# Kernel tuning notes

Hardware: AMD Instinct MI355X
Metric: run time of the kernel (lower is better)

The kernel has to match this reference:

```python
import jax, jax.numpy as jnp
import numpy as np

EPS = 1e-10


def setup_inputs() -> dict:
    key = jax.random.key(0)
    k1, k2, k3 = jax.random.split(key, 3)
    B, X, Y = 16, 512, 512
    predictions = jax.random.uniform(k1, (B, 5, X, Y), dtype=jnp.float32)
    inputs = jax.random.uniform(k2, (B, 3, X, Y), dtype=jnp.float32)
    heart = jax.random.randint(k3, (B, 1, X, Y), 0, 2, dtype=jnp.int32)
    return {"predictions": predictions, "inputs": inputs, "heart": heart}


def reference(predictions, inputs, heart):
    # predictions: [B,5,X,Y] soft class maps (chan 0 unused); inputs: [B,3,X,Y] MRI modalities
    # heart: [B,1,X,Y] binary ROI mask. Loops over b/k/m in the torch source are vectorized;
    # boolean-mask gathers become multiply-by-mask with masked reductions (same math).
    mask = (heart[:, 0] == 1).astype(predictions.dtype)          # [B,X,Y]
    pred = predictions[:, 1:5]                                   # [B,K=4,X,Y]
    inp = inputs                                                 # [B,M=3,X,Y]

    w = pred * mask[:, None]                                     # masked soft weights [B,K,X,Y]
    sw = jnp.sum(w, axis=(2, 3))                                 # [B,K]
    denom = sw[:, :, None] + EPS                                 # [B,K,1]

    # per-(k,m) weighted mean over masked pixels
    mu = jnp.einsum('bkxy,bmxy->bkm', w, inp) / denom            # [B,K,M]
    diff = inp[:, None, :, :, :] - mu[:, :, :, None, None]       # [B,K,M,X,Y]
    var = jnp.einsum('bkxy,bkmxy->bkm', w, diff * diff) / denom + EPS

    # Gaussian pdf per (k,m,pixel), scaled by pred_k (as in temp[k,m] = pred[k]*pdf)
    inv_norm = 1.0 / jnp.sqrt(2.0 * jnp.pi * var)                # [B,K,M]
    pdf = inv_norm[:, :, :, None, None] * jnp.exp(
        -(diff * diff) / (2.0 * var)[:, :, :, None, None])      # [B,K,M,X,Y]
    temp = pred[:, :, None] * pdf                                # [B,K,M,X,Y]

    mix = jnp.sum(jnp.prod(temp, axis=2), axis=1)                # [B,X,Y]
    loglik = jnp.log(mix + EPS)                                  # [B,X,Y]

    # masked mean over ROI pixels per batch (== torch.mean over gathered pixels)
    per_b = -jnp.sum(loglik * mask, axis=(1, 2)) / jnp.sum(mask, axis=(1, 2))
    return jnp.mean(per_b)
```

## Files before the change

kernel.cpp:

```cpp
#include <hip/hip_runtime.h>
#include <math.h>

constexpr int NB = 16;
constexpr int XY = 512 * 512;
constexpr int NV = XY / 4;
constexpr int G  = 128;

constexpr int P1OFF = 4096;

__device__ __forceinline__ float waveReduce64(float v) {
#pragma unroll
    for (int off = 32; off > 0; off >>= 1) v += __shfl_down(v, off, 64);
    return v;
}

__device__ __forceinline__ float rfl(float x) {
    return __uint_as_float(__builtin_amdgcn_readfirstlane(__float_as_uint(x)));
}

#define PIX1(h_, e0_, e1_, e2_, p0_, p1_, p2_, p3_) do {                      \
    float mm_ = ((h_) == 1) ? 1.f : 0.f;                                      \
    cnt += mm_;                                                               \
    float w0_ = (p0_) * mm_, w1_ = (p1_) * mm_, w2_ = (p2_) * mm_,            \
          w3_ = (p3_) * mm_;                                                  \
    s0_0 += w0_; s0_1 += w1_; s0_2 += w2_; s0_3 += w3_;                       \
    float t_;                                                                 \
    t_ = w0_ * (e0_); u00 += t_; q00 = fmaf(t_, (e0_), q00);                  \
    t_ = w0_ * (e1_); u01 += t_; q01 = fmaf(t_, (e1_), q01);                  \
    t_ = w0_ * (e2_); u02 += t_; q02 = fmaf(t_, (e2_), q02);                  \
    t_ = w1_ * (e0_); u10 += t_; q10 = fmaf(t_, (e0_), q10);                  \
    t_ = w1_ * (e1_); u11 += t_; q11 = fmaf(t_, (e1_), q11);                  \
    t_ = w1_ * (e2_); u12 += t_; q12 = fmaf(t_, (e2_), q12);                  \
    t_ = w2_ * (e0_); u20 += t_; q20 = fmaf(t_, (e0_), q20);                  \
    t_ = w2_ * (e1_); u21 += t_; q21 = fmaf(t_, (e1_), q21);                  \
    t_ = w2_ * (e2_); u22 += t_; q22 = fmaf(t_, (e2_), q22);                  \
    t_ = w3_ * (e0_); u30 += t_; q30 = fmaf(t_, (e0_), q30);                  \
    t_ = w3_ * (e1_); u31 += t_; q31 = fmaf(t_, (e1_), q31);                  \
    t_ = w3_ * (e2_); u32 += t_; q32 = fmaf(t_, (e2_), q32);                  \
} while (0)

#define RED(i_, var_) { float r_ = waveReduce64(var_); if (lane == 0) sh[wav][i_] = r_; }

#define PARAMK(K_, mu0_, mu1_, mu2_, h0_, h1_, h2_, C_) {                     \
    double S0_ = tot[1 + (K_)];                                               \
    double den_ = S0_ + 1e-10;                                                \
    double Cd_ = 1.0;                                                         \
    double S1_, S2_, muv_, var_;                                              \
    S1_ = tot[5 + (K_)*3 + 0]; S2_ = tot[17 + (K_)*3 + 0];                    \
    muv_ = S1_ / den_;                                                        \
    var_ = (S2_ - 2.0 * muv_ * S1_ + muv_ * muv_ * S0_) / den_ + 1e-10;       \
    mu0_ = (float)muv_; h0_ = (float)(0.5 / var_);                            \
    Cd_ *= 1.0 / sqrt(6.283185307179586 * var_);                              \
    S1_ = tot[5 + (K_)*3 + 1]; S2_ = tot[17 + (K_)*3 + 1];                    \
    muv_ = S1_ / den_;                                                        \
    var_ = (S2_ - 2.0 * muv_ * S1_ + muv_ * muv_ * S0_) / den_ + 1e-10;       \
    mu1_ = (float)muv_; h1_ = (float)(0.5 / var_);                            \
    Cd_ *= 1.0 / sqrt(6.283185307179586 * var_);                              \
    S1_ = tot[5 + (K_)*3 + 2]; S2_ = tot[17 + (K_)*3 + 2];                    \
    muv_ = S1_ / den_;                                                        \
    var_ = (S2_ - 2.0 * muv_ * S1_ + muv_ * muv_ * S0_) / den_ + 1e-10;       \
    mu2_ = (float)muv_; h2_ = (float)(0.5 / var_);                            \
    Cd_ *= 1.0 / sqrt(6.283185307179586 * var_);                              \
    C_ = (float)Cd_;                                                          \
}

#define PIX2(h_, e0_, e1_, e2_, p0_, p1_, p2_, p3_) do {                      \
    float m_ = ((h_) == 1) ? 1.f : 0.f;                                       \
    float d0_, d1_, d2_, ex_, pc_;                                            \
    float mix_;                                                               \
    d0_ = (e0_) - mu00; d1_ = (e1_) - mu01; d2_ = (e2_) - mu02;               \
    ex_ = fmaf(d0_ * d0_, hv00, fmaf(d1_ * d1_, hv01, d2_ * d2_ * hv02));     \
    pc_ = (p0_) * (p0_) * (p0_);                                              \
    mix_ = C0 * pc_ * __expf(-ex_);                                           \
    d0_ = (e0_) - mu10; d1_ = (e1_) - mu11; d2_ = (e2_) - mu12;               \
    ex_ = fmaf(d0_ * d0_, hv10, fmaf(d1_ * d1_, hv11, d2_ * d2_ * hv12));     \
    pc_ = (p1_) * (p1_) * (p1_);                                              \
    mix_ = fmaf(C1 * pc_, __expf(-ex_), mix_);                                \
    d0_ = (e0_) - mu20; d1_ = (e1_) - mu21; d2_ = (e2_) - mu22;               \
    ex_ = fmaf(d0_ * d0_, hv20, fmaf(d1_ * d1_, hv21, d2_ * d2_ * hv22));     \
    pc_ = (p2_) * (p2_) * (p2_);                                              \
    mix_ = fmaf(C2 * pc_, __expf(-ex_), mix_);                                \
    d0_ = (e0_) - mu30; d1_ = (e1_) - mu31; d2_ = (e2_) - mu32;               \
    ex_ = fmaf(d0_ * d0_, hv30, fmaf(d1_ * d1_, hv31, d2_ * d2_ * hv32));     \
    pc_ = (p3_) * (p3_) * (p3_);                                              \
    mix_ = fmaf(C3 * pc_, __expf(-ex_), mix_);                                \
    lacc += m_ * __logf(mix_ + 1e-10f);                                       \
} while (0)

#define LOADSET1(S, v_)                                                       \
    int4   h##S  = H[v_];                                                     \
    float4 f0##S = I0[v_], f1##S = I1[v_], f2##S = I2[v_];                    \
    float4 g0##S = P1[v_], g1##S = P2[v_], g2##S = P3[v_], g3##S = P4[v_];

#define PIXSET1(S)                                                            \
    PIX1(h##S.x, f0##S.x, f1##S.x, f2##S.x, g0##S.x, g1##S.x, g2##S.x, g3##S.x); \
    PIX1(h##S.y, f0##S.y, f1##S.y, f2##S.y, g0##S.y, g1##S.y, g2##S.y, g3##S.y); \
    PIX1(h##S.z, f0##S.z, f1##S.z, f2##S.z, g0##S.z, g1##S.z, g2##S.z, g3##S.z); \
    PIX1(h##S.w, f0##S.w, f1##S.w, f2##S.w, g0##S.w, g1##S.w, g2##S.w, g3##S.w);

#define PIXSET2(S)                                                            \
    PIX2(h##S.x, f0##S.x, f1##S.x, f2##S.x, g0##S.x, g1##S.x, g2##S.x, g3##S.x); \
    PIX2(h##S.y, f0##S.y, f1##S.y, f2##S.y, g0##S.y, g1##S.y, g2##S.y, g3##S.y); \
    PIX2(h##S.z, f0##S.z, f1##S.z, f2##S.z, g0##S.z, g1##S.z, g2##S.z, g3##S.z); \
    PIX2(h##S.w, f0##S.w, f1##S.w, f2##S.w, g0##S.w, g1##S.w, g2##S.w, g3##S.w);

#define DECL_PTRS                                                             \
    const float4* P1 = reinterpret_cast<const float4*>(predictions + (size_t)b * 5 * XY + 1 * XY); \
    const float4* P2 = reinterpret_cast<const float4*>(predictions + (size_t)b * 5 * XY + 2 * XY); \
    const float4* P3 = reinterpret_cast<const float4*>(predictions + (size_t)b * 5 * XY + 3 * XY); \
    const float4* P4 = reinterpret_cast<const float4*>(predictions + (size_t)b * 5 * XY + 4 * XY); \
    const float4* I0 = reinterpret_cast<const float4*>(inputs + (size_t)b * 3 * XY + 0 * XY); \
    const float4* I1 = reinterpret_cast<const float4*>(inputs + (size_t)b * 3 * XY + 1 * XY); \
    const float4* I2 = reinterpret_cast<const float4*>(inputs + (size_t)b * 3 * XY + 2 * XY); \
    const int4*   H  = reinterpret_cast<const int4*>(heart + (size_t)b * XY);

__global__ __launch_bounds__(256, 2) void pass1_moments(
        const float* __restrict__ predictions,
        const float* __restrict__ inputs,
        const int*   __restrict__ heart,
        char*        __restrict__ wsraw) {
    const int b   = blockIdx.y;
    const int g   = blockIdx.x;
    const int tid = threadIdx.x;
    DECL_PTRS;

    float cnt = 0.f;
    float s0_0 = 0.f, s0_1 = 0.f, s0_2 = 0.f, s0_3 = 0.f;
    float u00 = 0.f, u01 = 0.f, u02 = 0.f, u10 = 0.f, u11 = 0.f, u12 = 0.f;
    float u20 = 0.f, u21 = 0.f, u22 = 0.f, u30 = 0.f, u31 = 0.f, u32 = 0.f;
    float q00 = 0.f, q01 = 0.f, q02 = 0.f, q10 = 0.f, q11 = 0.f, q12 = 0.f;
    float q20 = 0.f, q21 = 0.f, q22 = 0.f, q30 = 0.f, q31 = 0.f, q32 = 0.f;

    const int vA = g * 256 + tid;
    const int vB = vA + G * 256;

    LOADSET1(A, vA);
    LOADSET1(B, vB);
    __builtin_amdgcn_sched_barrier(0);
    PIXSET1(A);
    PIXSET1(B);

    __shared__ float sh[4][29];
    const int lane = tid & 63;
    const int wav  = tid >> 6;
    RED(0, cnt);
    RED(1, s0_0); RED(2, s0_1); RED(3, s0_2); RED(4, s0_3);
    RED(5, u00); RED(6, u01); RED(7, u02);
    RED(8, u10); RED(9, u11); RED(10, u12);
    RED(11, u20); RED(12, u21); RED(13, u22);
    RED(14, u30); RED(15, u31); RED(16, u32);
    RED(17, q00); RED(18, q01); RED(19, q02);
    RED(20, q10); RED(21, q11); RED(22, q12);
    RED(23, q20); RED(24, q21); RED(25, q22);
    RED(26, q30); RED(27, q31); RED(28, q32);
    __syncthreads();

    float* p1 = reinterpret_cast<float*>(wsraw + P1OFF);
    if (tid < 29) {
        float v = sh[0][tid] + sh[1][tid] + sh[2][tid] + sh[3][tid];
        p1[(((size_t)b * G + g) << 5) + tid] = v;
    }
}

__global__ __launch_bounds__(256) void reduce_totals(char* __restrict__ wsraw) {
    const int b   = blockIdx.x;
    const int tid = threadIdx.x;
    const float* p1 = reinterpret_cast<const float*>(wsraw + P1OFF) + ((size_t)b * G << 5);
    __shared__ double red[8][32];
    const int col = tid & 31, r = tid >> 5;
    double s = 0.0;
    if (col < 29) {
#pragma unroll
        for (int j = r; j < G; j += 8) s += (double)p1[((size_t)j << 5) + col];
    }
    red[r][col] = s;
    __syncthreads();
    if (tid < 29) {
        double t = 0.0;
#pragma unroll
        for (int r2 = 0; r2 < 8; ++r2) t += red[r2][tid];
        reinterpret_cast<double*>(wsraw)[(size_t)b * 32 + tid] = t;
    }
}

__global__ __launch_bounds__(256, 2) void pass2_loglik(
        const float* __restrict__ predictions,
        const float* __restrict__ inputs,
        const int*   __restrict__ heart,
        char*        __restrict__ wsraw) {
    const int b   = blockIdx.y;
    const int g   = blockIdx.x;
    const int tid = threadIdx.x;
    const double* tot = reinterpret_cast<const double*>(wsraw) + (size_t)b * 32;

    float mu00, mu01, mu02, mu10, mu11, mu12, mu20, mu21, mu22, mu30, mu31, mu32;
    float hv00, hv01, hv02, hv10, hv11, hv12, hv20, hv21, hv22, hv30, hv31, hv32;
    float C0, C1, C2, C3;
    PARAMK(0, mu00, mu01, mu02, hv00, hv01, hv02, C0);
    PARAMK(1, mu10, mu11, mu12, hv10, hv11, hv12, C1);
    PARAMK(2, mu20, mu21, mu22, hv20, hv21, hv22, C2);
    PARAMK(3, mu30, mu31, mu32, hv30, hv31, hv32, C3);
    mu00=rfl(mu00); mu01=rfl(mu01); mu02=rfl(mu02);
    mu10=rfl(mu10); mu11=rfl(mu11); mu12=rfl(mu12);
    mu20=rfl(mu20); mu21=rfl(mu21); mu22=rfl(mu22);
    mu30=rfl(mu30); mu31=rfl(mu31); mu32=rfl(mu32);
    hv00=rfl(hv00); hv01=rfl(hv01); hv02=rfl(hv02);
    hv10=rfl(hv10); hv11=rfl(hv11); hv12=rfl(hv12);
    hv20=rfl(hv20); hv21=rfl(hv21); hv22=rfl(hv22);
    hv30=rfl(hv30); hv31=rfl(hv31); hv32=rfl(hv32);
    C0=rfl(C0); C1=rfl(C1); C2=rfl(C2); C3=rfl(C3);

    DECL_PTRS;

    float lacc = 0.f;
    const int vA = g * 256 + tid;
    const int vB = vA + G * 256;

    LOADSET1(A, vA);
    LOADSET1(B, vB);
    __builtin_amdgcn_sched_barrier(0);
    PIXSET2(A);
    PIXSET2(B);

    __shared__ float sh2[4];
    const int lane = tid & 63;
    const int wav  = tid >> 6;
    {
        float v = waveReduce64(lacc);
        if (lane == 0) sh2[wav] = v;
    }
    __syncthreads();
    if (tid == 0) {
        float* p1 = reinterpret_cast<float*>(wsraw + P1OFF);
        p1[(((size_t)b * G + g) << 5) + 29] = sh2[0] + sh2[1] + sh2[2] + sh2[3];
    }
}

__global__ __launch_bounds__(256) void finalize_kernel(
        const char* __restrict__ wsraw, float* __restrict__ out) {
    const float*  p1  = reinterpret_cast<const float*>(wsraw + P1OFF);
    const double* tot = reinterpret_cast<const double*>(wsraw);
    __shared__ double red[16][17];
    const int tid = threadIdx.x;
    const int b = tid >> 4, r = tid & 15;
    double s = 0.0;
#pragma unroll
    for (int j = r; j < G; j += 16)
        s += (double)p1[(((size_t)b * G + j) << 5) + 29];
    red[b][r] = s;
    __syncthreads();
    double v = 0.0;
    if (tid < NB) {
        double l = 0.0;
#pragma unroll
        for (int r2 = 0; r2 < 16; ++r2) l += red[tid][r2];
        v = -l / tot[(size_t)tid * 32];
    }
#pragma unroll
    for (int off = 8; off > 0; off >>= 1) v += __shfl_down(v, off, 64);
    if (tid == 0) out[0] = (float)(v / (double)NB);
}

extern "C" void kernel_launch(void* const* d_in, const int* in_sizes, int n_in,
                              void* d_out, int out_size, void* d_ws, size_t ws_size,
                              hipStream_t stream) {
    const float* predictions = (const float*)d_in[0];
    const float* inputs      = (const float*)d_in[1];
    const int*   heart       = (const int*)d_in[2];
    float* out   = (float*)d_out;
    char*  wsraw = (char*)d_ws;

    pass1_moments<<<dim3(G, NB), 256, 0, stream>>>(predictions, inputs, heart, wsraw);
    reduce_totals<<<dim3(NB),    256, 0, stream>>>(wsraw);
    pass2_loglik <<<dim3(G, NB), 256, 0, stream>>>(predictions, inputs, heart, wsraw);
    finalize_kernel<<<1,         256, 0, stream>>>(wsraw, out);
}
```

Measured before the change: 202.3 us.

## Split pass1 moments per class across waves and loop pass2 over fewer blocks

Pass 1 now gives each wavefront a single class k, so it accumulates only 7 moments instead of 29. That cuts register pressure and shared-memory reductions, at the cost of every wave reloading the inputs and mask, so those are read four times per block. Pass 2 moves from two fixed loads per thread to a strided loop over 64 blocks per batch. Its partials go to a separate workspace region, and the launch-bound occupancy hints are dropped.

```diff
diff --git a/kernel.cpp b/kernel.cpp
--- a/kernel.cpp
+++ b/kernel.cpp
@@ -4,9 +4,14 @@
 constexpr int NB = 16;
 constexpr int XY = 512 * 512;
 constexpr int NV = XY / 4;
-constexpr int G  = 128;
+
+constexpr int G1 = 128;
+constexpr int NIT1 = NV / (G1 * 64);
+constexpr int G2 = 64;
+constexpr int NIT2 = NV / (G2 * 256);
 
 constexpr int P1OFF = 4096;
+constexpr int P2OFF = P1OFF + NB * G1 * 32 * 4;
 
 __device__ __forceinline__ float waveReduce64(float v) {
 #pragma unroll
@@ -18,28 +23,16 @@
     return __uint_as_float(__builtin_amdgcn_readfirstlane(__float_as_uint(x)));
 }
 
-#define PIX1(h_, e0_, e1_, e2_, p0_, p1_, p2_, p3_) do {                      \
+#define PIXW(h_, p_, e0_, e1_, e2_) do {                                      \
     float mm_ = ((h_) == 1) ? 1.f : 0.f;                                      \
     cnt += mm_;                                                               \
-    float w0_ = (p0_) * mm_, w1_ = (p1_) * mm_, w2_ = (p2_) * mm_,            \
-          w3_ = (p3_) * mm_;                                                  \
-    s0_0 += w0_; s0_1 += w1_; s0_2 += w2_; s0_3 += w3_;                       \
+    float w_ = (p_) * mm_;                                                    \
+    s0 += w_;                                                                 \
     float t_;                                                                 \
-    t_ = w0_ * (e0_); u00 += t_; q00 = fmaf(t_, (e0_), q00);                  \
-    t_ = w0_ * (e1_); u01 += t_; q01 = fmaf(t_, (e1_), q01);                  \
-    t_ = w0_ * (e2_); u02 += t_; q02 = fmaf(t_, (e2_), q02);                  \
-    t_ = w1_ * (e0_); u10 += t_; q10 = fmaf(t_, (e0_), q10);                  \
-    t_ = w1_ * (e1_); u11 += t_; q11 = fmaf(t_, (e1_), q11);                  \
-    t_ = w1_ * (e2_); u12 += t_; q12 = fmaf(t_, (e2_), q12);                  \
-    t_ = w2_ * (e0_); u20 += t_; q20 = fmaf(t_, (e0_), q20);                  \
-    t_ = w2_ * (e1_); u21 += t_; q21 = fmaf(t_, (e1_), q21);                  \
-    t_ = w2_ * (e2_); u22 += t_; q22 = fmaf(t_, (e2_), q22);                  \
-    t_ = w3_ * (e0_); u30 += t_; q30 = fmaf(t_, (e0_), q30);                  \
-    t_ = w3_ * (e1_); u31 += t_; q31 = fmaf(t_, (e1_), q31);                  \
-    t_ = w3_ * (e2_); u32 += t_; q32 = fmaf(t_, (e2_), q32);                  \
+    t_ = w_ * (e0_); u0 += t_; q0 = fmaf(t_, (e0_), q0);                      \
+    t_ = w_ * (e1_); u1 += t_; q1 = fmaf(t_, (e1_), q1);                      \
+    t_ = w_ * (e2_); u2 += t_; q2 = fmaf(t_, (e2_), q2);                      \
 } while (0)
-
-#define RED(i_, var_) { float r_ = waveReduce64(var_); if (lane == 0) sh[wav][i_] = r_; }
 
 #define PARAMK(K_, mu0_, mu1_, mu2_, h0_, h1_, h2_, C_) {                     \
     double S0_ = tot[1 + (K_)];                                               \
@@ -87,91 +80,68 @@
     lacc += m_ * __logf(mix_ + 1e-10f);                                       \
 } while (0)
 
-#define LOADSET1(S, v_)                                                       \
-    int4   h##S  = H[v_];                                                     \
-    float4 f0##S = I0[v_], f1##S = I1[v_], f2##S = I2[v_];                    \
-    float4 g0##S = P1[v_], g1##S = P2[v_], g2##S = P3[v_], g3##S = P4[v_];
-
-#define PIXSET1(S)                                                            \
-    PIX1(h##S.x, f0##S.x, f1##S.x, f2##S.x, g0##S.x, g1##S.x, g2##S.x, g3##S.x); \
-    PIX1(h##S.y, f0##S.y, f1##S.y, f2##S.y, g0##S.y, g1##S.y, g2##S.y, g3##S.y); \
-    PIX1(h##S.z, f0##S.z, f1##S.z, f2##S.z, g0##S.z, g1##S.z, g2##S.z, g3##S.z); \
-    PIX1(h##S.w, f0##S.w, f1##S.w, f2##S.w, g0##S.w, g1##S.w, g2##S.w, g3##S.w);
-
-#define PIXSET2(S)                                                            \
-    PIX2(h##S.x, f0##S.x, f1##S.x, f2##S.x, g0##S.x, g1##S.x, g2##S.x, g3##S.x); \
-    PIX2(h##S.y, f0##S.y, f1##S.y, f2##S.y, g0##S.y, g1##S.y, g2##S.y, g3##S.y); \
-    PIX2(h##S.z, f0##S.z, f1##S.z, f2##S.z, g0##S.z, g1##S.z, g2##S.z, g3##S.z); \
-    PIX2(h##S.w, f0##S.w, f1##S.w, f2##S.w, g0##S.w, g1##S.w, g2##S.w, g3##S.w);
-
-#define DECL_PTRS                                                             \
-    const float4* P1 = reinterpret_cast<const float4*>(predictions + (size_t)b * 5 * XY + 1 * XY); \
-    const float4* P2 = reinterpret_cast<const float4*>(predictions + (size_t)b * 5 * XY + 2 * XY); \
-    const float4* P3 = reinterpret_cast<const float4*>(predictions + (size_t)b * 5 * XY + 3 * XY); \
-    const float4* P4 = reinterpret_cast<const float4*>(predictions + (size_t)b * 5 * XY + 4 * XY); \
-    const float4* I0 = reinterpret_cast<const float4*>(inputs + (size_t)b * 3 * XY + 0 * XY); \
-    const float4* I1 = reinterpret_cast<const float4*>(inputs + (size_t)b * 3 * XY + 1 * XY); \
-    const float4* I2 = reinterpret_cast<const float4*>(inputs + (size_t)b * 3 * XY + 2 * XY); \
-    const int4*   H  = reinterpret_cast<const int4*>(heart + (size_t)b * XY);
-
-__global__ __launch_bounds__(256, 2) void pass1_moments(
+__global__ __launch_bounds__(256) void pass1_moments(
         const float* __restrict__ predictions,
         const float* __restrict__ inputs,
         const int*   __restrict__ heart,
         char*        __restrict__ wsraw) {
-    const int b   = blockIdx.y;
-    const int g   = blockIdx.x;
-    const int tid = threadIdx.x;
-    DECL_PTRS;
-
-    float cnt = 0.f;
-    float s0_0 = 0.f, s0_1 = 0.f, s0_2 = 0.f, s0_3 = 0.f;
-    float u00 = 0.f, u01 = 0.f, u02 = 0.f, u10 = 0.f, u11 = 0.f, u12 = 0.f;
-    float u20 = 0.f, u21 = 0.f, u22 = 0.f, u30 = 0.f, u31 = 0.f, u32 = 0.f;
-    float q00 = 0.f, q01 = 0.f, q02 = 0.f, q10 = 0.f, q11 = 0.f, q12 = 0.f;
-    float q20 = 0.f, q21 = 0.f, q22 = 0.f, q30 = 0.f, q31 = 0.f, q32 = 0.f;
-
-    const int vA = g * 256 + tid;
-    const int vB = vA + G * 256;
-
-    LOADSET1(A, vA);
-    LOADSET1(B, vB);
-    __builtin_amdgcn_sched_barrier(0);
-    PIXSET1(A);
-    PIXSET1(B);
-
-    __shared__ float sh[4][29];
+    const int b    = blockIdx.y;
+    const int g    = blockIdx.x;
+    const int tid  = threadIdx.x;
     const int lane = tid & 63;
     const int wav  = tid >> 6;
-    RED(0, cnt);
-    RED(1, s0_0); RED(2, s0_1); RED(3, s0_2); RED(4, s0_3);
-    RED(5, u00); RED(6, u01); RED(7, u02);
-    RED(8, u10); RED(9, u11); RED(10, u12);
-    RED(11, u20); RED(12, u21); RED(13, u22);
-    RED(14, u30); RED(15, u31); RED(16, u32);
-    RED(17, q00); RED(18, q01); RED(19, q02);
-    RED(20, q10); RED(21, q11); RED(22, q12);
-    RED(23, q20); RED(24, q21); RED(25, q22);
-    RED(26, q30); RED(27, q31); RED(28, q32);
-    __syncthreads();
-
-    float* p1 = reinterpret_cast<float*>(wsraw + P1OFF);
-    if (tid < 29) {
-        float v = sh[0][tid] + sh[1][tid] + sh[2][tid] + sh[3][tid];
-        p1[(((size_t)b * G + g) << 5) + tid] = v;
+
+    const float4* PK = reinterpret_cast<const float4*>(
+        predictions + (size_t)b * 5 * XY + (size_t)(1 + wav) * XY);
+    const float4* I0 = reinterpret_cast<const float4*>(inputs + (size_t)b * 3 * XY + 0 * XY);
+    const float4* I1 = reinterpret_cast<const float4*>(inputs + (size_t)b * 3 * XY + 1 * XY);
+    const float4* I2 = reinterpret_cast<const float4*>(inputs + (size_t)b * 3 * XY + 2 * XY);
+    const int4*   H  = reinterpret_cast<const int4*>(heart + (size_t)b * XY);
+
+    float cnt = 0.f, s0 = 0.f;
+    float u0 = 0.f, u1 = 0.f, u2 = 0.f;
+    float q0 = 0.f, q1 = 0.f, q2 = 0.f;
+
+#pragma unroll 4
+    for (int it = 0; it < NIT1; ++it) {
+        const int v = g * 64 + lane + it * (G1 * 64);
+        int4   h  = H[v];
+        float4 pk = PK[v];
+        float4 f0 = I0[v], f1 = I1[v], f2 = I2[v];
+        PIXW(h.x, pk.x, f0.x, f1.x, f2.x);
+        PIXW(h.y, pk.y, f0.y, f1.y, f2.y);
+        PIXW(h.z, pk.z, f0.z, f1.z, f2.z);
+        PIXW(h.w, pk.w, f0.w, f1.w, f2.w);
+    }
+
+    s0 = waveReduce64(s0);
+    u0 = waveReduce64(u0); u1 = waveReduce64(u1); u2 = waveReduce64(u2);
+    q0 = waveReduce64(q0); q1 = waveReduce64(q1); q2 = waveReduce64(q2);
+    if (wav == 0) cnt = waveReduce64(cnt);
+
+    if (lane == 0) {
+        float* dst = reinterpret_cast<float*>(wsraw + P1OFF) + (((size_t)b * G1 + g) << 5);
+        dst[1 + wav]           = s0;
+        dst[5 + 3 * wav + 0]   = u0;
+        dst[5 + 3 * wav + 1]   = u1;
+        dst[5 + 3 * wav + 2]   = u2;
+        dst[17 + 3 * wav + 0]  = q0;
+        dst[17 + 3 * wav + 1]  = q1;
+        dst[17 + 3 * wav + 2]  = q2;
+        if (wav == 0) dst[0]   = cnt;
     }
 }
 
 __global__ __launch_bounds__(256) void reduce_totals(char* __restrict__ wsraw) {
     const int b   = blockIdx.x;
     const int tid = threadIdx.x;
-    const float* p1 = reinterpret_cast<const float*>(wsraw + P1OFF) + ((size_t)b * G << 5);
+    const float* p1 = reinterpret_cast<const float*>(wsraw + P1OFF) + ((size_t)b * G1 << 5);
     __shared__ double red[8][32];
     const int col = tid & 31, r = tid >> 5;
     double s = 0.0;
     if (col < 29) {
 #pragma unroll
-        for (int j = r; j < G; j += 8) s += (double)p1[((size_t)j << 5) + col];
+        for (int j = r; j < G1; j += 8) s += (double)p1[((size_t)j << 5) + col];
     }
     red[r][col] = s;
     __syncthreads();
@@ -183,7 +153,7 @@
     }
 }
 
-__global__ __launch_bounds__(256, 2) void pass2_loglik(
+__global__ __launch_bounds__(256) void pass2_loglik(
         const float* __restrict__ predictions,
         const float* __restrict__ inputs,
         const int*   __restrict__ heart,
@@ -210,17 +180,27 @@
     hv30=rfl(hv30); hv31=rfl(hv31); hv32=rfl(hv32);
     C0=rfl(C0); C1=rfl(C1); C2=rfl(C2); C3=rfl(C3);
 
-    DECL_PTRS;
+    const float4* P1 = reinterpret_cast<const float4*>(predictions + (size_t)b * 5 * XY + 1 * XY);
+    const float4* P2 = reinterpret_cast<const float4*>(predictions + (size_t)b * 5 * XY + 2 * XY);
+    const float4* P3 = reinterpret_cast<const float4*>(predictions + (size_t)b * 5 * XY + 3 * XY);
+    const float4* P4 = reinterpret_cast<const float4*>(predictions + (size_t)b * 5 * XY + 4 * XY);
+    const float4* I0 = reinterpret_cast<const float4*>(inputs + (size_t)b * 3 * XY + 0 * XY);
+    const float4* I1 = reinterpret_cast<const float4*>(inputs + (size_t)b * 3 * XY + 1 * XY);
+    const float4* I2 = reinterpret_cast<const float4*>(inputs + (size_t)b * 3 * XY + 2 * XY);
+    const int4*   H  = reinterpret_cast<const int4*>(heart + (size_t)b * XY);
 
     float lacc = 0.f;
-    const int vA = g * 256 + tid;
-    const int vB = vA + G * 256;
-
-    LOADSET1(A, vA);
-    LOADSET1(B, vB);
-    __builtin_amdgcn_sched_barrier(0);
-    PIXSET2(A);
-    PIXSET2(B);
+#pragma unroll 2
+    for (int it = 0; it < NIT2; ++it) {
+        const int v = g * 256 + tid + it * (G2 * 256);
+        int4   h  = H[v];
+        float4 f0 = I0[v], f1 = I1[v], f2 = I2[v];
+        float4 g0 = P1[v], g1 = P2[v], g2 = P3[v], g3 = P4[v];
+        PIX2(h.x, f0.x, f1.x, f2.x, g0.x, g1.x, g2.x, g3.x);
+        PIX2(h.y, f0.y, f1.y, f2.y, g0.y, g1.y, g2.y, g3.y);
+        PIX2(h.z, f0.z, f1.z, f2.z, g0.z, g1.z, g2.z, g3.z);
+        PIX2(h.w, f0.w, f1.w, f2.w, g0.w, g1.w, g2.w, g3.w);
+    }
 
     __shared__ float sh2[4];
     const int lane = tid & 63;
@@ -231,22 +211,22 @@
     }
     __syncthreads();
     if (tid == 0) {
-        float* p1 = reinterpret_cast<float*>(wsraw + P1OFF);
-        p1[(((size_t)b * G + g) << 5) + 29] = sh2[0] + sh2[1] + sh2[2] + sh2[3];
+        float* p2 = reinterpret_cast<float*>(wsraw + P2OFF);
+        p2[(size_t)b * G2 + g] = sh2[0] + sh2[1] + sh2[2] + sh2[3];
     }
 }
 
 __global__ __launch_bounds__(256) void finalize_kernel(
         const char* __restrict__ wsraw, float* __restrict__ out) {
-    const float*  p1  = reinterpret_cast<const float*>(wsraw + P1OFF);
+    const float*  p2  = reinterpret_cast<const float*>(wsraw + P2OFF);
     const double* tot = reinterpret_cast<const double*>(wsraw);
     __shared__ double red[16][17];
     const int tid = threadIdx.x;
     const int b = tid >> 4, r = tid & 15;
     double s = 0.0;
 #pragma unroll
-    for (int j = r; j < G; j += 16)
-        s += (double)p1[(((size_t)b * G + j) << 5) + 29];
+    for (int j = r; j < G2; j += 16)
+        s += (double)p2[(size_t)b * G2 + j];
     red[b][r] = s;
     __syncthreads();
     double v = 0.0;
@@ -270,8 +250,8 @@
     float* out   = (float*)d_out;
     char*  wsraw = (char*)d_ws;
 
-    pass1_moments<<<dim3(G, NB), 256, 0, stream>>>(predictions, inputs, heart, wsraw);
-    reduce_totals<<<dim3(NB),    256, 0, stream>>>(wsraw);
-    pass2_loglik <<<dim3(G, NB), 256, 0, stream>>>(predictions, inputs, heart, wsraw);
-    finalize_kernel<<<1,         256, 0, stream>>>(wsraw, out);
-}
+    pass1_moments<<<dim3(G1, NB), 256, 0, stream>>>(predictions, inputs, heart, wsraw);
+    reduce_totals<<<dim3(NB),     256, 0, stream>>>(wsraw);
+    pass2_loglik <<<dim3(G2, NB), 256, 0, stream>>>(predictions, inputs, heart, wsraw);
+    finalize_kernel<<<1,          256, 0, stream>>>(wsraw, out);
+}
```

After: 195.0 us. 3.6% less time.

## Materialize packed fp16 per-pixel intermediate in pass1 and read it in pass2

Applied to the files above, without the earlier changes.

Pass1 now also writes a 16-byte packed half-precision record per pixel: masked cubed predictions, the three inputs, and the mask. Pass2 then streams only that record instead of re-reading the eight original fp32 planes, and uses a new grid size with a loop over 16 vectors per thread. The aim is to cut pass2's global read volume and skip recomputing the cubes, possibly serving the intermediate from the last-level cache. In exchange it adds write traffic in pass1 and loses precision from rounding inputs and weights to fp16.

```diff
diff --git a/kernel.cpp b/kernel.cpp
--- a/kernel.cpp
+++ b/kernel.cpp
@@ -1,12 +1,18 @@
 #include <hip/hip_runtime.h>
+#include <hip/hip_fp16.h>
 #include <math.h>
+#include <stdint.h>
 
 constexpr int NB = 16;
 constexpr int XY = 512 * 512;
 constexpr int NV = XY / 4;
-constexpr int G  = 128;
-
-constexpr int P1OFF = 4096;
+
+constexpr int G1 = 128;
+constexpr int G2 = 64;
+
+constexpr int    P1OFF  = 4096;
+constexpr int    P2OFF  = P1OFF + NB * G1 * 32 * 4;
+constexpr size_t IMDOFF = 524288;
 
 __device__ __forceinline__ float waveReduce64(float v) {
 #pragma unroll
@@ -16,6 +22,30 @@
 
 __device__ __forceinline__ float rfl(float x) {
     return __uint_as_float(__builtin_amdgcn_readfirstlane(__float_as_uint(x)));
+}
+
+__device__ __forceinline__ unsigned pk2(float a, float b) {
+    union { __half2 h; unsigned u; } cv;
+    cv.h = __floats2half2_rn(a, b);
+    return cv.u;
+}
+__device__ __forceinline__ float2 up2(unsigned u) {
+    union { unsigned u; __half2 h; } cv;
+    cv.u = u;
+    return __half22float2(cv.h);
+}
+
+__device__ __forceinline__ uint4 packpix(int hh, float e0, float e1, float e2,
+                                         float p0, float p1, float p2, float p3) {
+    float mm = (hh == 1) ? 1.f : 0.f;
+    float c0 = p0 * p0 * p0 * mm, c1 = p1 * p1 * p1 * mm;
+    float c2 = p2 * p2 * p2 * mm, c3 = p3 * p3 * p3 * mm;
+    uint4 r;
+    r.x = pk2(c0, c1);
+    r.y = pk2(c2, c3);
+    r.z = pk2(e0, e1);
+    r.w = pk2(e2, mm);
+    return r;
 }
 
 #define PIX1(h_, e0_, e1_, e2_, p0_, p1_, p2_, p3_) do {                      \
@@ -64,57 +94,29 @@
     C_ = (float)Cd_;                                                          \
 }
 
-#define PIX2(h_, e0_, e1_, e2_, p0_, p1_, p2_, p3_) do {                      \
-    float m_ = ((h_) == 1) ? 1.f : 0.f;                                       \
-    float d0_, d1_, d2_, ex_, pc_;                                            \
+#define PIX2P(q_) do {                                                        \
+    float2 a01_ = up2((q_).x);                                                \
+    float2 a23_ = up2((q_).y);                                                \
+    float2 e01_ = up2((q_).z);                                                \
+    float2 e2m_ = up2((q_).w);                                                \
+    float d0_, d1_, d2_, ex_;                                                 \
     float mix_;                                                               \
-    d0_ = (e0_) - mu00; d1_ = (e1_) - mu01; d2_ = (e2_) - mu02;               \
+    d0_ = e01_.x - mu00; d1_ = e01_.y - mu01; d2_ = e2m_.x - mu02;            \
     ex_ = fmaf(d0_ * d0_, hv00, fmaf(d1_ * d1_, hv01, d2_ * d2_ * hv02));     \
-    pc_ = (p0_) * (p0_) * (p0_);                                              \
-    mix_ = C0 * pc_ * __expf(-ex_);                                           \
-    d0_ = (e0_) - mu10; d1_ = (e1_) - mu11; d2_ = (e2_) - mu12;               \
+    mix_ = C0 * a01_.x * __expf(-ex_);                                        \
+    d0_ = e01_.x - mu10; d1_ = e01_.y - mu11; d2_ = e2m_.x - mu12;            \
     ex_ = fmaf(d0_ * d0_, hv10, fmaf(d1_ * d1_, hv11, d2_ * d2_ * hv12));     \
-    pc_ = (p1_) * (p1_) * (p1_);                                              \
-    mix_ = fmaf(C1 * pc_, __expf(-ex_), mix_);                                \
-    d0_ = (e0_) - mu20; d1_ = (e1_) - mu21; d2_ = (e2_) - mu22;               \
+    mix_ = fmaf(C1 * a01_.y, __expf(-ex_), mix_);                             \
+    d0_ = e01_.x - mu20; d1_ = e01_.y - mu21; d2_ = e2m_.x - mu22;            \
     ex_ = fmaf(d0_ * d0_, hv20, fmaf(d1_ * d1_, hv21, d2_ * d2_ * hv22));     \
-    pc_ = (p2_) * (p2_) * (p2_);                                              \
-    mix_ = fmaf(C2 * pc_, __expf(-ex_), mix_);                                \
-    d0_ = (e0_) - mu30; d1_ = (e1_) - mu31; d2_ = (e2_) - mu32;               \
+    mix_ = fmaf(C2 * a23_.x, __expf(-ex_), mix_);                             \
+    d0_ = e01_.x - mu30; d1_ = e01_.y - mu31; d2_ = e2m_.x - mu32;            \
     ex_ = fmaf(d0_ * d0_, hv30, fmaf(d1_ * d1_, hv31, d2_ * d2_ * hv32));     \
-    pc_ = (p3_) * (p3_) * (p3_);                                              \
-    mix_ = fmaf(C3 * pc_, __expf(-ex_), mix_);                                \
-    lacc += m_ * __logf(mix_ + 1e-10f);                                       \
+    mix_ = fmaf(C3 * a23_.y, __expf(-ex_), mix_);                             \
+    lacc += e2m_.y * __logf(mix_ + 1e-10f);                                   \
 } while (0)
 
-#define LOADSET1(S, v_)                                                       \
-    int4   h##S  = H[v_];                                                     \
-    float4 f0##S = I0[v_], f1##S = I1[v_], f2##S = I2[v_];                    \
-    float4 g0##S = P1[v_], g1##S = P2[v_], g2##S = P3[v_], g3##S = P4[v_];
-
-#define PIXSET1(S)                                                            \
-    PIX1(h##S.x, f0##S.x, f1##S.x, f2##S.x, g0##S.x, g1##S.x, g2##S.x, g3##S.x); \
-    PIX1(h##S.y, f0##S.y, f1##S.y, f2##S.y, g0##S.y, g1##S.y, g2##S.y, g3##S.y); \
-    PIX1(h##S.z, f0##S.z, f1##S.z, f2##S.z, g0##S.z, g1##S.z, g2##S.z, g3##S.z); \
-    PIX1(h##S.w, f0##S.w, f1##S.w, f2##S.w, g0##S.w, g1##S.w, g2##S.w, g3##S.w);
-
-#define PIXSET2(S)                                                            \
-    PIX2(h##S.x, f0##S.x, f1##S.x, f2##S.x, g0##S.x, g1##S.x, g2##S.x, g3##S.x); \
-    PIX2(h##S.y, f0##S.y, f1##S.y, f2##S.y, g0##S.y, g1##S.y, g2##S.y, g3##S.y); \
-    PIX2(h##S.z, f0##S.z, f1##S.z, f2##S.z, g0##S.z, g1##S.z, g2##S.z, g3##S.z); \
-    PIX2(h##S.w, f0##S.w, f1##S.w, f2##S.w, g0##S.w, g1##S.w, g2##S.w, g3##S.w);
-
-#define DECL_PTRS                                                             \
-    const float4* P1 = reinterpret_cast<const float4*>(predictions + (size_t)b * 5 * XY + 1 * XY); \
-    const float4* P2 = reinterpret_cast<const float4*>(predictions + (size_t)b * 5 * XY + 2 * XY); \
-    const float4* P3 = reinterpret_cast<const float4*>(predictions + (size_t)b * 5 * XY + 3 * XY); \
-    const float4* P4 = reinterpret_cast<const float4*>(predictions + (size_t)b * 5 * XY + 4 * XY); \
-    const float4* I0 = reinterpret_cast<const float4*>(inputs + (size_t)b * 3 * XY + 0 * XY); \
-    const float4* I1 = reinterpret_cast<const float4*>(inputs + (size_t)b * 3 * XY + 1 * XY); \
-    const float4* I2 = reinterpret_cast<const float4*>(inputs + (size_t)b * 3 * XY + 2 * XY); \
-    const int4*   H  = reinterpret_cast<const int4*>(heart + (size_t)b * XY);
-
-__global__ __launch_bounds__(256, 2) void pass1_moments(
+__global__ __launch_bounds__(256) void pass1_moments(
         const float* __restrict__ predictions,
         const float* __restrict__ inputs,
         const int*   __restrict__ heart,
@@ -122,7 +124,16 @@
     const int b   = blockIdx.y;
     const int g   = blockIdx.x;
     const int tid = threadIdx.x;
-    DECL_PTRS;
+
+    const float4* P1 = reinterpret_cast<const float4*>(predictions + (size_t)b * 5 * XY + 1 * XY);
+    const float4* P2 = reinterpret_cast<const float4*>(predictions + (size_t)b * 5 * XY + 2 * XY);
+    const float4* P3 = reinterpret_cast<const float4*>(predictions + (size_t)b * 5 * XY + 3 * XY);
+    const float4* P4 = reinterpret_cast<const float4*>(predictions + (size_t)b * 5 * XY + 4 * XY);
+    const float4* I0 = reinterpret_cast<const float4*>(inputs + (size_t)b * 3 * XY + 0 * XY);
+    const float4* I1 = reinterpret_cast<const float4*>(inputs + (size_t)b * 3 * XY + 1 * XY);
+    const float4* I2 = reinterpret_cast<const float4*>(inputs + (size_t)b * 3 * XY + 2 * XY);
+    const int4*   H  = reinterpret_cast<const int4*>(heart + (size_t)b * XY);
+    uint4* imd = reinterpret_cast<uint4*>(wsraw + IMDOFF) + (size_t)b * XY;
 
     float cnt = 0.f;
     float s0_0 = 0.f, s0_1 = 0.f, s0_2 = 0.f, s0_3 = 0.f;
@@ -131,14 +142,22 @@
     float q00 = 0.f, q01 = 0.f, q02 = 0.f, q10 = 0.f, q11 = 0.f, q12 = 0.f;
     float q20 = 0.f, q21 = 0.f, q22 = 0.f, q30 = 0.f, q31 = 0.f, q32 = 0.f;
 
-    const int vA = g * 256 + tid;
-    const int vB = vA + G * 256;
-
-    LOADSET1(A, vA);
-    LOADSET1(B, vB);
-    __builtin_amdgcn_sched_barrier(0);
-    PIXSET1(A);
-    PIXSET1(B);
+#pragma unroll
+    for (int it = 0; it < 2; ++it) {
+        const int v = g * 256 + tid + it * (G1 * 256);
+        int4   h  = H[v];
+        float4 f0 = I0[v], f1 = I1[v], f2 = I2[v];
+        float4 g0 = P1[v], g1 = P2[v], g2 = P3[v], g3 = P4[v];
+        PIX1(h.x, f0.x, f1.x, f2.x, g0.x, g1.x, g2.x, g3.x);
+        PIX1(h.y, f0.y, f1.y, f2.y, g0.y, g1.y, g2.y, g3.y);
+        PIX1(h.z, f0.z, f1.z, f2.z, g0.z, g1.z, g2.z, g3.z);
+        PIX1(h.w, f0.w, f1.w, f2.w, g0.w, g1.w, g2.w, g3.w);
+        uint4* w = imd + 4 * (size_t)v;
+        w[0] = packpix(h.x, f0.x, f1.x, f2.x, g0.x, g1.x, g2.x, g3.x);
+        w[1] = packpix(h.y, f0.y, f1.y, f2.y, g0.y, g1.y, g2.y, g3.y);
+        w[2] = packpix(h.z, f0.z, f1.z, f2.z, g0.z, g1.z, g2.z, g3.z);
+        w[3] = packpix(h.w, f0.w, f1.w, f2.w, g0.w, g1.w, g2.w, g3.w);
+    }
 
     __shared__ float sh[4][29];
     const int lane = tid & 63;
@@ -154,24 +173,23 @@
     RED(23, q20); RED(24, q21); RED(25, q22);
     RED(26, q30); RED(27, q31); RED(28, q32);
     __syncthreads();
-
-    float* p1 = reinterpret_cast<float*>(wsraw + P1OFF);
     if (tid < 29) {
         float v = sh[0][tid] + sh[1][tid] + sh[2][tid] + sh[3][tid];
-        p1[(((size_t)b * G + g) << 5) + tid] = v;
+        float* p1 = reinterpret_cast<float*>(wsraw + P1OFF);
+        p1[(((size_t)b * G1 + g) << 5) + tid] = v;
     }
 }
 
 __global__ __launch_bounds__(256) void reduce_totals(char* __restrict__ wsraw) {
     const int b   = blockIdx.x;
     const int tid = threadIdx.x;
-    const float* p1 = reinterpret_cast<const float*>(wsraw + P1OFF) + ((size_t)b * G << 5);
+    const float* p1 = reinterpret_cast<const float*>(wsraw + P1OFF) + ((size_t)b * G1 << 5);
     __shared__ double red[8][32];
     const int col = tid & 31, r = tid >> 5;
     double s = 0.0;
     if (col < 29) {
 #pragma unroll
-        for (int j = r; j < G; j += 8) s += (double)p1[((size_t)j << 5) + col];
+        for (int j = r; j < G1; j += 8) s += (double)p1[((size_t)j << 5) + col];
     }
     red[r][col] = s;
     __syncthreads();
@@ -183,11 +201,8 @@
     }
 }
 
-__global__ __launch_bounds__(256, 2) void pass2_loglik(
-        const float* __restrict__ predictions,
-        const float* __restrict__ inputs,
-        const int*   __restrict__ heart,
-        char*        __restrict__ wsraw) {
+__global__ __launch_bounds__(256) void pass2_loglik(
+        char* __restrict__ wsraw) {
     const int b   = blockIdx.y;
     const int g   = blockIdx.x;
     const int tid = threadIdx.x;
@@ -210,17 +225,14 @@
     hv30=rfl(hv30); hv31=rfl(hv31); hv32=rfl(hv32);
     C0=rfl(C0); C1=rfl(C1); C2=rfl(C2); C3=rfl(C3);
 
-    DECL_PTRS;
+    const uint4* imd = reinterpret_cast<const uint4*>(wsraw + IMDOFF) + (size_t)b * XY;
 
     float lacc = 0.f;
-    const int vA = g * 256 + tid;
-    const int vB = vA + G * 256;
-
-    LOADSET1(A, vA);
-    LOADSET1(B, vB);
-    __builtin_amdgcn_sched_barrier(0);
-    PIXSET2(A);
-    PIXSET2(B);
+#pragma unroll 4
+    for (int i = 0; i < 16; ++i) {
+        uint4 q = imd[(size_t)g * 4096 + i * 256 + tid];
+        PIX2P(q);
+    }
 
     __shared__ float sh2[4];
     const int lane = tid & 63;
@@ -231,22 +243,22 @@
     }
     __syncthreads();
     if (tid == 0) {
-        float* p1 = reinterpret_cast<float*>(wsraw + P1OFF);
-        p1[(((size_t)b * G + g) << 5) + 29] = sh2[0] + sh2[1] + sh2[2] + sh2[3];
+        float* p2 = reinterpret_cast<float*>(wsraw + P2OFF);
+        p2[(size_t)b * G2 + g] = sh2[0] + sh2[1] + sh2[2] + sh2[3];
     }
 }
 
 __global__ __launch_bounds__(256) void finalize_kernel(
         const char* __restrict__ wsraw, float* __restrict__ out) {
-    const float*  p1  = reinterpret_cast<const float*>(wsraw + P1OFF);
+    const float*  p2  = reinterpret_cast<const float*>(wsraw + P2OFF);
     const double* tot = reinterpret_cast<const double*>(wsraw);
     __shared__ double red[16][17];
     const int tid = threadIdx.x;
     const int b = tid >> 4, r = tid & 15;
     double s = 0.0;
 #pragma unroll
-    for (int j = r; j < G; j += 16)
-        s += (double)p1[(((size_t)b * G + j) << 5) + 29];
+    for (int j = r; j < G2; j += 16)
+        s += (double)p2[(size_t)b * G2 + j];
     red[b][r] = s;
     __syncthreads();
     double v = 0.0;
@@ -270,8 +282,8 @@
     float* out   = (float*)d_out;
     char*  wsraw = (char*)d_ws;
 
-    pass1_moments<<<dim3(G, NB), 256, 0, stream>>>(predictions, inputs, heart, wsraw);
-    reduce_totals<<<dim3(NB),    256, 0, stream>>>(wsraw);
-    pass2_loglik <<<dim3(G, NB), 256, 0, stream>>>(predictions, inputs, heart, wsraw);
-    finalize_kernel<<<1,         256, 0, stream>>>(wsraw, out);
-}
+    pass1_moments<<<dim3(G1, NB), 256, 0, stream>>>(predictions, inputs, heart, wsraw);
+    reduce_totals<<<dim3(NB),     256, 0, stream>>>(wsraw);
+    pass2_loglik <<<dim3(G2, NB), 256, 0, stream>>>(wsraw);
+    finalize_kernel<<<1,          256, 0, stream>>>(wsraw, out);
+}
```

Result: no change. 206.2 us (+1.9%).
